# Kernel tuning notes

Measured on AMD Instinct MI355X. Metric: run time of the kernel, lower is better.

Reference implementation:

```python
import jax, jax.numpy as jnp
import numpy as np

N, E, F, R, L, B = 50000, 800000, 64, 20, 2, 64
RC = 5.0
ZMAX = 100
LN2 = 0.6931471805599453

def ssp(x):
    # shifted softplus: softplus(x) - log(2)
    return jax.nn.softplus(x) - LN2

def setup_inputs() -> dict:
    key = jax.random.key(0)
    ks = jax.random.split(key, 32)
    w = lambda i, shape: jax.random.normal(ks[i], shape, dtype=jnp.float32) * 0.05
    inp = {
        'z': jax.random.randint(ks[0], (N,), 0, ZMAX + 1),
        'pos': jax.random.normal(ks[1], (N, 3), dtype=jnp.float32) * 3.0,
        'edge_index': jax.random.randint(ks[2], (2, E), 0, N),
        'batch_idx': jnp.sort(jax.random.randint(ks[3], (N,), 0, B)),
        'emb': jax.random.normal(ks[4], (ZMAX + 1, F), dtype=jnp.float32),
        'phi_W': w(5, (L, 3 * F, F)), 'phi_b': w(6, (L, 3 * F)),
        'filt_W1': w(7, (L, F, R)), 'filt_b1': w(8, (L, F)),
        'filt_W2': w(9, (L, 3 * F, F)), 'filt_b2': w(10, (L, 3 * F)),
        'U_W': w(11, (L, F, F)), 'V_W': w(12, (L, F, F)),
        'a_W1': w(13, (L, F, 2 * F)), 'a_b1': w(14, (L, F)),
        'a_W2': w(15, (L, 3 * F, F)), 'a_b2': w(16, (L, 3 * F)),
        'e_W1': w(17, (F // 2, F)), 'e_b1': w(18, (F // 2,)),
        'e_W2': w(19, (1, F // 2)), 'e_b2': w(20, (1,)),
        'dip_w': w(21, (F,)),
    }
    return inp

def reference(z, pos, edge_index, batch_idx, emb, phi_W, phi_b,
              filt_W1, filt_b1, filt_W2, filt_b2, U_W, V_W,
              a_W1, a_b1, a_W2, a_b2, e_W1, e_b1, e_W2, e_b2, dip_w):
    src, dst = edge_index[0], edge_index[1]
    s = emb[z]                               # (N, F)
    v = jnp.zeros((N, F, 3), dtype=s.dtype)  # (N, F, 3)

    # edge geometry
    r_vec = pos[dst] - pos[src]              # (E, 3)
    r_norm = jnp.linalg.norm(r_vec, axis=-1)
    r_hat = r_vec / jnp.maximum(r_norm, 1e-8)[:, None]
    # Gaussian RBF on [0, RC], widths = grid spacing
    mu = jnp.linspace(0.0, RC, R, dtype=s.dtype)
    width = mu[1] - mu[0]
    e_ij = jnp.exp(-((r_norm[:, None] - mu[None, :]) ** 2) / (2.0 * width * width))
    fc = 0.5 * (jnp.cos(jnp.pi * r_norm / RC) + 1.0) * (r_norm < RC)
    e_ij = e_ij * fc[:, None]                # (E, R)

    for l in range(L):
        # message block
        filt = ssp(e_ij @ filt_W1[l].T + filt_b1[l]) @ filt_W2[l].T + filt_b2[l]  # (E, 3F)
        W_s, W_v, W_r = jnp.split(filt, 3, axis=-1)
        phi = s[dst] @ phi_W[l].T + phi_b[l]                                       # (E, 3F)
        phi_s, phi_v, phi_r = jnp.split(phi, 3, axis=-1)
        m_s = W_s * phi_s                                                          # (E, F)
        m_v = W_v[:, :, None] * v[dst] + (W_r * phi_r)[:, :, None] * r_hat[:, None, :]  # (E, F, 3)
        s = s + jax.ops.segment_sum(m_s, src, num_segments=N)
        v = v + jax.ops.segment_sum(m_v, src, num_segments=N)
        # update block
        Uv = jnp.einsum('nfd,gf->ngd', v, U_W[l])
        Vv = jnp.einsum('nfd,gf->ngd', v, V_W[l])
        Vv_norm_sq = jnp.sum(Vv * Vv, axis=-1)                                     # (N, F)
        a = ssp(jnp.concatenate([s, Vv_norm_sq], axis=-1) @ a_W1[l].T + a_b1[l]) @ a_W2[l].T + a_b2[l]
        a_ss, a_sv, a_vv = jnp.split(a, 3, axis=-1)
        inner = jnp.sum(Uv * Vv, axis=-1)
        s = s + a_ss + a_sv * inner
        v = v + a_vv[:, :, None] * Uv

    # heads
    eps_i = (ssp(s @ e_W1.T + e_b1) @ e_W2.T + e_b2)[:, 0]  # (N,)
    energy = jax.ops.segment_sum(eps_i, batch_idx, num_segments=B)
    mu_i = jnp.sum(v * dip_w[None, :, None], axis=1)         # (N, 3)
    mu_mol = jax.ops.segment_sum(mu_i, batch_idx, num_segments=B)
    dipole = jnp.linalg.norm(mu_mol, axis=-1)
    charges = jnp.zeros((N,), dtype=s.dtype)
    return energy, dipole, charges
```

## Files before the change

### kernel.cpp

```cpp
#include <hip/hip_runtime.h>
#include <math.h>

static constexpr int N  = 50000;
static constexpr int E  = 800000;
static constexpr int F  = 64;
static constexpr int R  = 20;
static constexpr int NL = 2;
static constexpr int B  = 64;
static constexpr float RC   = 5.0f;
static constexpr float LN2F = 0.6931471805599453f;
static constexpr float WIDTH  = RC / (R - 1);
static constexpr float INV2W2 = 1.0f / (2.0f * WIDTH * WIDTH);
static constexpr float PI_F = 3.14159265358979323846f;

static constexpr int   NB     = 4096;
static constexpr float DR     = RC / NB;
static constexpr float INV_DR = NB / RC;
static constexpr int   TROWS  = NB + 2;
static constexpr int   TENT   = NB + 1;

static constexpr int NBLK_SCAN = (N + 255) / 256;

typedef __attribute__((ext_vector_type(8))) short bf16x8;
typedef __attribute__((ext_vector_type(4))) float f32x4;
typedef __attribute__((ext_vector_type(3))) unsigned uint32x3;

__device__ __forceinline__ float ssp_f(float x) {
    return fmaxf(x, 0.0f) + log1pf(__expf(-fabsf(x))) - LN2F;
}

__device__ __forceinline__ short f2bf(float x) {
    unsigned u = __builtin_bit_cast(unsigned, x);
    unsigned r = (u + 0x7fffu + ((u >> 16) & 1u)) >> 16;
    return (short)r;
}
__device__ __forceinline__ float bf_lo(unsigned u) {
    return __builtin_bit_cast(float, u << 16);
}
__device__ __forceinline__ float bf_hi(unsigned u) {
    return __builtin_bit_cast(float, u & 0xffff0000u);
}

__global__ void k_hist(const int* __restrict__ ei, int* __restrict__ cnt) {
    int e = blockIdx.x * blockDim.x + threadIdx.x;
    if (e < E) atomicAdd(&cnt[ei[e]], 1);
}

__global__ void k_scan_a(const int* __restrict__ cnt, int* __restrict__ bsum) {
    __shared__ int part[256];
    const int t = threadIdx.x;
    const int idx = blockIdx.x * 256 + t;
    int v = (idx < N) ? cnt[idx] : 0;
    part[t] = v;
    __syncthreads();
    for (int d = 1; d < 256; d <<= 1) {
        int x = (t >= d) ? part[t - d] : 0;
        __syncthreads();
        part[t] += x;
        __syncthreads();
    }
    if (t == 255) bsum[blockIdx.x] = part[255];
}

__global__ void k_scan_b(const int* __restrict__ bsum, int* __restrict__ bpre,
                         int* __restrict__ offN) {
    __shared__ int part[256];
    const int t = threadIdx.x;
    int v = (t < NBLK_SCAN) ? bsum[t] : 0;
    part[t] = v;
    __syncthreads();
    for (int d = 1; d < 256; d <<= 1) {
        int x = (t >= d) ? part[t - d] : 0;
        __syncthreads();
        part[t] += x;
        __syncthreads();
    }
    if (t < NBLK_SCAN) bpre[t] = part[t] - v;
    if (t == NBLK_SCAN - 1) *offN = part[t];
}

__global__ void k_scan_c(const int* __restrict__ cnt, const int* __restrict__ bpre,
                         int* __restrict__ off, int* __restrict__ cur) {
    __shared__ int part[256];
    const int t = threadIdx.x;
    const int idx = blockIdx.x * 256 + t;
    int v = (idx < N) ? cnt[idx] : 0;
    part[t] = v;
    __syncthreads();
    for (int d = 1; d < 256; d <<= 1) {
        int x = (t >= d) ? part[t - d] : 0;
        __syncthreads();
        part[t] += x;
        __syncthreads();
    }
    if (idx < N) {
        int e = bpre[blockIdx.x] + part[t] - v;
        off[idx] = e;
        cur[idx] = e;
    }
}

__global__ void k_scatter(const int* __restrict__ ei, int* __restrict__ cur,
                          const float* __restrict__ pos, uint4* __restrict__ edata) {
    int e = blockIdx.x * blockDim.x + threadIdx.x;
    if (e >= E) return;
    int src = ei[e], dst = ei[E + e];
    int p = atomicAdd(&cur[src], 1);
    float qx = pos[dst * 3 + 0] - pos[src * 3 + 0];
    float qy = pos[dst * 3 + 1] - pos[src * 3 + 1];
    float qz = pos[dst * 3 + 2] - pos[src * 3 + 2];
    float rn = sqrtf(qx * qx + qy * qy + qz * qz);
    float invn = 1.0f / fmaxf(rn, 1e-8f);
    float t = rn * INV_DR;
    int i = (int)t;
    float fr = t - (float)i;
    if (i >= NB) { i = NB; fr = 0.0f; }
    uint4 rec;
    rec.x = (unsigned)dst;
    rec.y = (unsigned)i | ((unsigned)(unsigned short)f2bf(fr) << 16);
    rec.z = (unsigned)(unsigned short)f2bf(qx * invn)
          | ((unsigned)(unsigned short)f2bf(qy * invn) << 16);
    rec.w = (unsigned)(unsigned short)f2bf(qz * invn);
    edata[p] = rec;
}

__global__ void k_table(const float* __restrict__ fW1, const float* __restrict__ fb1,
                        const float* __restrict__ fW2, const float* __restrict__ fb2,
                        unsigned short* __restrict__ Tp) {
    const int l   = blockIdx.x / TROWS;
    const int row = blockIdx.x % TROWS;
    const int lane = threadIdx.x;
    const float r = fminf((float)row, (float)NB) * DR;
    const float fc = (r < RC) ? 0.5f * (__cosf(PI_F * r * (1.0f / RC)) + 1.0f) : 0.0f;

    __shared__ float sh[F];
    float acc = fb1[l * F + lane];
    const float* w1 = fW1 + (size_t)l * F * R + (size_t)lane * R;
    #pragma unroll
    for (int rr = 0; rr < R; rr++) {
        float dmu = r - rr * WIDTH;
        float er = __expf(-dmu * dmu * INV2W2) * fc;
        acc = fmaf(er, w1[rr], acc);
    }
    sh[lane] = ssp_f(acc);
    __syncthreads();
    unsigned short* TpL = Tp + (size_t)l * TENT * 384;
    #pragma unroll
    for (int p = 0; p < 3; p++) {
        int c = p * 64 + lane;
        float a = fb2[l * 192 + c];
        const float* w2 = fW2 + ((size_t)l * 192 + c) * 64;
        #pragma unroll 8
        for (int k = 0; k < F; k++) a = fmaf(sh[k], w2[k], a);
        unsigned short bf = (unsigned short)f2bf(a);
        if (row <= NB) TpL[(size_t)row * 384 + lane * 6 + p * 2 + 0] = bf;
        if (row >= 1)  TpL[(size_t)(row - 1) * 384 + lane * 6 + p * 2 + 1] = bf;
    }
}

__launch_bounds__(256)
__global__ void k_pack0(float* __restrict__ s, const int* __restrict__ z,
                        const float* __restrict__ emb,
                        const float* __restrict__ PW, const float* __restrict__ Pb,
                        unsigned* __restrict__ ndAV) {
    __shared__ float sbuf[4][F];
    const int lane = threadIdx.x & 63;
    const int wid  = threadIdx.x >> 6;
    const int gwave = blockIdx.x * 4 + wid;
    const int nwaves = gridDim.x * 4;

    float wsr[F], wrr[F];
    {
        const float* rs = PW + (size_t)lane * 64;
        const float* rr = PW + (size_t)(128 + lane) * 64;
        #pragma unroll
        for (int k = 0; k < F; k += 4) {
            float4 a = *(const float4*)(rs + k);
            wsr[k] = a.x; wsr[k+1] = a.y; wsr[k+2] = a.z; wsr[k+3] = a.w;
            float4 b = *(const float4*)(rr + k);
            wrr[k] = b.x; wrr[k+1] = b.y; wrr[k+2] = b.z; wrr[k+3] = b.w;
        }
    }
    const float bs = Pb[lane], br = Pb[128 + lane];

    for (int n = gwave; n < N; n += nwaves) {
        float sv = emb[(size_t)z[n] * F + lane];
        s[(size_t)n * F + lane] = sv;
        sbuf[wid][lane] = sv;
        float as = bs, ar = br;
        #pragma unroll
        for (int k = 0; k < F; k += 4) {
            float4 s4 = *(const float4*)&sbuf[wid][k];
            as = fmaf(s4.x, wsr[k],   as); as = fmaf(s4.y, wsr[k+1], as);
            as = fmaf(s4.z, wsr[k+2], as); as = fmaf(s4.w, wsr[k+3], as);
            ar = fmaf(s4.x, wrr[k],   ar); ar = fmaf(s4.y, wrr[k+1], ar);
            ar = fmaf(s4.z, wrr[k+2], ar); ar = fmaf(s4.w, wrr[k+3], ar);
        }
        ndAV[((size_t)n * 64 + lane) * 3] =
              (unsigned)(unsigned short)f2bf(as)
            | ((unsigned)(unsigned short)f2bf(ar) << 16);
    }
}

__device__ __forceinline__ uint32x3 load_tbl(const unsigned short* __restrict__ TpL,
                                             unsigned edy, int lane) {
    const int i = (int)(edy & 0xffffu);
    return *(const uint32x3*)(TpL + (size_t)i * 384 + lane * 6);
}

template<bool ACCUMV>
__device__ __forceinline__ uint32x3 load_rec(const unsigned* __restrict__ ndAV,
                                             unsigned dst, int lane) {
    const unsigned* p = ndAV + ((size_t)dst * 64 + lane) * 3;
    uint32x3 r;
    if (ACCUMV) {
        r = *(const uint32x3*)p;
    } else {
        r.x = *p; r.y = 0; r.z = 0;
    }
    return r;
}

template<bool ACCUMV>
__device__ __forceinline__ void consume_edge(const uint4 ed, const uint32x3 t,
                                             const uint32x3 r,
                                             float& ms, float& mv0, float& mv1, float& mv2) {
    const float fr = bf_hi(ed.y);
    const float Ws = fmaf(fr, bf_hi(t.x) - bf_lo(t.x), bf_lo(t.x));
    const float Wr = fmaf(fr, bf_hi(t.z) - bf_lo(t.z), bf_lo(t.z));
    ms = fmaf(Ws, bf_lo(r.x), ms);
    const float c = Wr * bf_hi(r.x);
    const float rhx = bf_lo(ed.z), rhy = bf_hi(ed.z), rhz = bf_lo(ed.w);
    if (ACCUMV) {
        const float Wv = fmaf(fr, bf_hi(t.y) - bf_lo(t.y), bf_lo(t.y));
        mv0 = fmaf(Wv, bf_lo(r.y), fmaf(c, rhx, mv0));
        mv1 = fmaf(Wv, bf_hi(r.y), fmaf(c, rhy, mv1));
        mv2 = fmaf(Wv, bf_lo(r.z), fmaf(c, rhz, mv2));
    } else {
        mv0 = fmaf(c, rhx, mv0);
        mv1 = fmaf(c, rhy, mv1);
        mv2 = fmaf(c, rhz, mv2);
    }
}

template<bool ACCUMV>
__launch_bounds__(256, 8)
__global__ void k_gather(const uint4* __restrict__ edata, const int* __restrict__ off,
                         const unsigned short* __restrict__ TpL,
                         const unsigned* __restrict__ ndAV,
                         float* __restrict__ s, float* __restrict__ v) {
    __shared__ float red[4][4][64];
    const int lane = threadIdx.x & 63;
    const int wv   = threadIdx.x >> 6;
    const int n = blockIdx.x;
    const int base = off[n], end = off[n + 1];

    float ms = 0.f, mv0 = 0.f, mv1 = 0.f, mv2 = 0.f;
    int kc = base + wv;
    if (kc < end) {
        uint4 edC = edata[kc];
        int kn = kc + 4;
        bool hasN = kn < end;
        uint4 edN = edC;
        if (hasN) edN = edata[kn];
        uint32x3 tC = load_tbl(TpL, edC.y, lane);
        uint32x3 rC = load_rec<ACCUMV>(ndAV, edC.x, lane);
        for (;;) {
            const int kn2 = kn + 4;
            const bool hasN2 = hasN && (kn2 < end);
            uint4 edN2 = edC;
            if (hasN2) edN2 = edata[kn2];
            uint32x3 tN = tC, rN = rC;
            if (hasN) {
                tN = load_tbl(TpL, edN.y, lane);
                rN = load_rec<ACCUMV>(ndAV, edN.x, lane);
            }
            consume_edge<ACCUMV>(edC, tC, rC, ms, mv0, mv1, mv2);
            if (!hasN) break;
            edC = edN; tC = tN; rC = rN;
            edN = edN2; hasN = hasN2; kn = kn2;
        }
    }
    red[wv][0][lane] = ms;
    red[wv][1][lane] = mv0;
    red[wv][2][lane] = mv1;
    red[wv][3][lane] = mv2;
    __syncthreads();
    if (wv == 0) {
        ms  = red[0][0][lane] + red[1][0][lane] + red[2][0][lane] + red[3][0][lane];
        mv0 = red[0][1][lane] + red[1][1][lane] + red[2][1][lane] + red[3][1][lane];
        mv1 = red[0][2][lane] + red[1][2][lane] + red[2][2][lane] + red[3][2][lane];
        mv2 = red[0][3][lane] + red[1][3][lane] + red[2][3][lane] + red[3][3][lane];
        s[(size_t)n * F + lane] += ms;
        float* vo = v + (size_t)n * 3 * F + lane;
        if (ACCUMV) {
            vo[0]     += mv0;
            vo[F]     += mv1;
            vo[2 * F] += mv2;
        } else {
            vo[0] = mv0; vo[F] = mv1; vo[2 * F] = mv2;
        }
    }
}

__device__ __forceinline__ bf16x8 load_wfrag(const float* __restrict__ Wp, int ldk,
                                             int nrow, int k0) {
    const float* p = Wp + (size_t)nrow * ldk + k0;
    float4 a = *(const float4*)p;
    float4 b = *(const float4*)(p + 4);
    bf16x8 r;
    r[0] = f2bf(a.x); r[1] = f2bf(a.y); r[2] = f2bf(a.z); r[3] = f2bf(a.w);
    r[4] = f2bf(b.x); r[5] = f2bf(b.y); r[6] = f2bf(b.z); r[7] = f2bf(b.w);
    return r;
}

template<bool DO_PACK>
__launch_bounds__(256)
__global__ void k_update_mfma(float* __restrict__ s, float* __restrict__ v,
                              const float* __restrict__ U_W, const float* __restrict__ V_W,
                              const float* __restrict__ aW1, const float* __restrict__ ab1,
                              const float* __restrict__ aW2, const float* __restrict__ ab2,
                              const float* __restrict__ PW, const float* __restrict__ Pb,
                              unsigned* __restrict__ ndAV) {
    __shared__ short vlds[96 * 72];
    __shared__ short xlds[32 * 136];
    __shared__ short hlds[32 * 72];

    const int tid = threadIdx.x;
    const int l   = tid & 63;
    const int w   = tid >> 6;
    const int lo  = l & 15;
    const int hi  = l >> 4;

    bf16x8 ufr[2], vfr[2], w1fr[4], w2fr[3][2];
    #pragma unroll
    for (int kk = 0; kk < 2; kk++) {
        ufr[kk] = load_wfrag(U_W, 64, w * 16 + lo, kk * 32 + hi * 8);
        vfr[kk] = load_wfrag(V_W, 64, w * 16 + lo, kk * 32 + hi * 8);
    }
    #pragma unroll
    for (int kk = 0; kk < 4; kk++)
        w1fr[kk] = load_wfrag(aW1, 128, w * 16 + lo, kk * 32 + hi * 8);
    #pragma unroll
    for (int p = 0; p < 3; p++)
        #pragma unroll
        for (int kk = 0; kk < 2; kk++)
            w2fr[p][kk] = load_wfrag(aW2, 64, p * 64 + w * 16 + lo, kk * 32 + hi * 8);

    bf16x8 pws[2], pwr[2];
    float pbs = 0.f, pbr = 0.f;
    if (DO_PACK) {
        #pragma unroll
        for (int kk = 0; kk < 2; kk++) {
            pws[kk] = load_wfrag(PW, 64, w * 16 + lo, kk * 32 + hi * 8);
            pwr[kk] = load_wfrag(PW, 64, 128 + w * 16 + lo, kk * 32 + hi * 8);
        }
        pbs = Pb[w * 16 + lo];
        pbr = Pb[128 + w * 16 + lo];
    }

    const float ab1c  = ab1[w * 16 + lo];
    const float ab2c0 = ab2[w * 16 + lo];
    const float ab2c1 = ab2[64 + w * 16 + lo];
    const float ab2c2 = ab2[128 + w * 16 + lo];
    const int g = w * 16 + lo;

    for (int half = 0; half < 2; half++) {
        const int n0 = blockIdx.x * 64 + half * 32;
        if (half) __syncthreads();

        for (int u = tid; u < 96 * 8; u += 256) {
            int row = u >> 3, oct = u & 7;
            int d = row >> 5, nn = row & 31;
            int n = min(n0 + nn, N - 1);
            const float* src = v + ((size_t)n * 3 + d) * 64 + oct * 8;
            float4 a = *(const float4*)src;
            float4 b = *(const float4*)(src + 4);
            bf16x8 t;
            t[0] = f2bf(a.x); t[1] = f2bf(a.y); t[2] = f2bf(a.z); t[3] = f2bf(a.w);
            t[4] = f2bf(b.x); t[5] = f2bf(b.y); t[6] = f2bf(b.z); t[7] = f2bf(b.w);
            *(bf16x8*)&vlds[row * 72 + oct * 8] = t;
        }
        for (int u = tid; u < 32 * 8; u += 256) {
            int nn = u >> 3, oct = u & 7;
            int n = min(n0 + nn, N - 1);
            const float* src = s + (size_t)n * 64 + oct * 8;
            float4 a = *(const float4*)src;
            float4 b = *(const float4*)(src + 4);
            bf16x8 t;
            t[0] = f2bf(a.x); t[1] = f2bf(a.y); t[2] = f2bf(a.z); t[3] = f2bf(a.w);
            t[4] = f2bf(b.x); t[5] = f2bf(b.y); t[6] = f2bf(b.z); t[7] = f2bf(b.w);
            *(bf16x8*)&xlds[nn * 136 + oct * 8] = t;
        }
        __syncthreads();

        f32x4 cu[6], cv[6];
        #pragma unroll
        for (int mt = 0; mt < 6; mt++) { cu[mt] = (f32x4)0.0f; cv[mt] = (f32x4)0.0f; }
        #pragma unroll
        for (int kk = 0; kk < 2; kk++) {
            #pragma unroll
            for (int mt = 0; mt < 6; mt++) {
                bf16x8 af = *(const bf16x8*)&vlds[(mt * 16 + lo) * 72 + kk * 32 + hi * 8];
                cu[mt] = __builtin_amdgcn_mfma_f32_16x16x32_bf16(af, ufr[kk], cu[mt], 0, 0, 0);
                cv[mt] = __builtin_amdgcn_mfma_f32_16x16x32_bf16(af, vfr[kk], cv[mt], 0, 0, 0);
            }
        }

        f32x4 inn[2];
        #pragma unroll
        for (int nt = 0; nt < 2; nt++) {
            #pragma unroll
            for (int r = 0; r < 4; r++) {
                float vs = 0.f, ii = 0.f;
                #pragma unroll
                for (int d = 0; d < 3; d++) {
                    float a = cu[d * 2 + nt][r], b = cv[d * 2 + nt][r];
                    vs = fmaf(b, b, vs);
                    ii = fmaf(a, b, ii);
                }
                inn[nt][r] = ii;
                int nl = nt * 16 + hi * 4 + r;
                xlds[nl * 136 + 64 + w * 16 + lo] = f2bf(vs);
            }
        }
        __syncthreads();

        f32x4 c2[2];
        c2[0] = (f32x4)0.0f; c2[1] = (f32x4)0.0f;
        #pragma unroll
        for (int kk = 0; kk < 4; kk++) {
            #pragma unroll
            for (int mt = 0; mt < 2; mt++) {
                bf16x8 af = *(const bf16x8*)&xlds[(mt * 16 + lo) * 136 + kk * 32 + hi * 8];
                c2[mt] = __builtin_amdgcn_mfma_f32_16x16x32_bf16(af, w1fr[kk], c2[mt], 0, 0, 0);
            }
        }
        #pragma unroll
        for (int mt = 0; mt < 2; mt++)
            #pragma unroll
            for (int r = 0; r < 4; r++) {
                float hv = ssp_f(c2[mt][r] + ab1c);
                hlds[(mt * 16 + hi * 4 + r) * 72 + w * 16 + lo] = f2bf(hv);
            }
        __syncthreads();

        f32x4 c3[2][3];
        #pragma unroll
        for (int mt = 0; mt < 2; mt++)
            #pragma unroll
            for (int p = 0; p < 3; p++) c3[mt][p] = (f32x4)0.0f;
        #pragma unroll
        for (int kk = 0; kk < 2; kk++) {
            #pragma unroll
            for (int mt = 0; mt < 2; mt++) {
                bf16x8 af = *(const bf16x8*)&hlds[(mt * 16 + lo) * 72 + kk * 32 + hi * 8];
                #pragma unroll
                for (int p = 0; p < 3; p++)
                    c3[mt][p] = __builtin_amdgcn_mfma_f32_16x16x32_bf16(af, w2fr[p][kk], c3[mt][p], 0, 0, 0);
            }
        }

        float snew[2][4];
        #pragma unroll
        for (int mt = 0; mt < 2; mt++) {
            #pragma unroll
            for (int r = 0; r < 4; r++) {
                int n = n0 + mt * 16 + hi * 4 + r;
                if (n >= N) { snew[mt][r] = 0.f; continue; }
                float a_ss = c3[mt][0][r] + ab2c0;
                float a_sv = c3[mt][1][r] + ab2c1;
                float a_vv = c3[mt][2][r] + ab2c2;
                size_t si = (size_t)n * 64 + g;
                float sn = s[si] + a_ss + a_sv * inn[mt][r];
                s[si] = sn;
                snew[mt][r] = sn;
                float vn[3];
                #pragma unroll
                for (int d = 0; d < 3; d++) {
                    size_t vi = ((size_t)n * 3 + d) * 64 + g;
                    vn[d] = v[vi] + a_vv * cu[d * 2 + mt][r];
                    v[vi] = vn[d];
                }
                if (DO_PACK) {
                    unsigned* pp = ndAV + ((size_t)n * 64 + g) * 3;
                    pp[1] = (unsigned)(unsigned short)f2bf(vn[0])
                          | ((unsigned)(unsigned short)f2bf(vn[1]) << 16);
                    pp[2] = (unsigned)(unsigned short)f2bf(vn[2]);
                }
            }
        }

        if (DO_PACK) {
            __syncthreads();
            #pragma unroll
            for (int mt = 0; mt < 2; mt++)
                #pragma unroll
                for (int r = 0; r < 4; r++)
                    hlds[(mt * 16 + hi * 4 + r) * 72 + g] = f2bf(snew[mt][r]);
            __syncthreads();

            f32x4 cs[2], cr[2];
            cs[0] = (f32x4)0.0f; cs[1] = (f32x4)0.0f;
            cr[0] = (f32x4)0.0f; cr[1] = (f32x4)0.0f;
            #pragma unroll
            for (int kk = 0; kk < 2; kk++) {
                #pragma unroll
                for (int mt = 0; mt < 2; mt++) {
                    bf16x8 af = *(const bf16x8*)&hlds[(mt * 16 + lo) * 72 + kk * 32 + hi * 8];
                    cs[mt] = __builtin_amdgcn_mfma_f32_16x16x32_bf16(af, pws[kk], cs[mt], 0, 0, 0);
                    cr[mt] = __builtin_amdgcn_mfma_f32_16x16x32_bf16(af, pwr[kk], cr[mt], 0, 0, 0);
                }
            }
            #pragma unroll
            for (int mt = 0; mt < 2; mt++) {
                #pragma unroll
                for (int r = 0; r < 4; r++) {
                    int n = n0 + mt * 16 + hi * 4 + r;
                    if (n >= N) continue;
                    ndAV[((size_t)n * 64 + g) * 3] =
                          (unsigned)(unsigned short)f2bf(cs[mt][r] + pbs)
                        | ((unsigned)(unsigned short)f2bf(cr[mt][r] + pbr) << 16);
                }
            }
        }
    }
}

__global__ void k_heads(const float* __restrict__ s, const float* __restrict__ v,
                        const int* __restrict__ batch_idx,
                        const float* __restrict__ eW1, const float* __restrict__ eb1,
                        const float* __restrict__ eW2, const float* __restrict__ eb2,
                        const float* __restrict__ dip_w,
                        float* __restrict__ eacc, float* __restrict__ macc) {
    __shared__ float se[B];
    __shared__ float sm[3][B];
    if (threadIdx.x < B) se[threadIdx.x] = 0.0f;
    if (threadIdx.x < 3 * B) sm[threadIdx.x >> 6][threadIdx.x & 63] = 0.0f;
    __syncthreads();
    int n = blockIdx.x * blockDim.x + threadIdx.x;
    if (n < N) {
        int b = batch_idx[n];
        float sr[F];
        #pragma unroll
        for (int f = 0; f < F; f += 4) {
            float4 t = *(const float4*)&s[(size_t)n * F + f];
            sr[f] = t.x; sr[f+1] = t.y; sr[f+2] = t.z; sr[f+3] = t.w;
        }
        float eps = eb2[0];
        for (int jj = 0; jj < F / 2; jj++) {
            float acc = eb1[jj];
            #pragma unroll
            for (int f = 0; f < F; f++)
                acc = fmaf(sr[f], eW1[jj * F + f], acc);
            eps = fmaf(eW2[jj], ssp_f(acc), eps);
        }
        atomicAdd(&se[b], eps);
        #pragma unroll
        for (int d = 0; d < 3; d++) {
            float m = 0.0f;
            #pragma unroll 8
            for (int f = 0; f < F; f++)
                m = fmaf(v[((size_t)n * 3 + d) * F + f], dip_w[f], m);
            atomicAdd(&sm[d][b], m);
        }
    }
    __syncthreads();
    if (threadIdx.x < B) atomicAdd(&eacc[threadIdx.x], se[threadIdx.x]);
    if (threadIdx.x >= B && threadIdx.x < 4 * B) {
        int d = (threadIdx.x >> 6) - 1, b = threadIdx.x & 63;
        atomicAdd(&macc[d * B + b], sm[d][b]);
    }
}

__global__ void k_final(const float* __restrict__ eacc, const float* __restrict__ macc,
                        float* __restrict__ out) {
    int b = threadIdx.x;
    if (b < B) {
        out[b] = eacc[b];
        float mx = macc[b], my = macc[B + b], mz = macc[2 * B + b];
        out[B + b] = sqrtf(mx * mx + my * my + mz * mz);
    }
}

extern "C" void kernel_launch(void* const* d_in, const int* in_sizes, int n_in,
                              void* d_out, int out_size, void* d_ws, size_t ws_size,
                              hipStream_t stream) {
    const int*   z     = (const int*)d_in[0];
    const float* pos   = (const float*)d_in[1];
    const int*   ei    = (const int*)d_in[2];
    const int*   bidx  = (const int*)d_in[3];
    const float* emb   = (const float*)d_in[4];
    const float* phi_W = (const float*)d_in[5];
    const float* phi_b = (const float*)d_in[6];
    const float* fW1   = (const float*)d_in[7];
    const float* fb1   = (const float*)d_in[8];
    const float* fW2   = (const float*)d_in[9];
    const float* fb2   = (const float*)d_in[10];
    const float* U_W   = (const float*)d_in[11];
    const float* V_W   = (const float*)d_in[12];
    const float* aW1   = (const float*)d_in[13];
    const float* ab1   = (const float*)d_in[14];
    const float* aW2   = (const float*)d_in[15];
    const float* ab2   = (const float*)d_in[16];
    const float* eW1   = (const float*)d_in[17];
    const float* eb1   = (const float*)d_in[18];
    const float* eW2   = (const float*)d_in[19];
    const float* eb2   = (const float*)d_in[20];
    const float* dip_w = (const float*)d_in[21];
    float* out = (float*)d_out;

    float* ws = (float*)d_ws;
    float* s    = ws;
    float* v    = s + (size_t)N * F;
    unsigned* ndAV = (unsigned*)(v + (size_t)N * F * 3);
    unsigned short* Tp = (unsigned short*)(ndAV + (size_t)N * 64 * 3);
    float* eacc = (float*)(Tp + (size_t)NL * TENT * 384);
    float* macc = eacc + B;
    int*   cnt  = (int*)(macc + 3 * B);
    int*   off  = cnt  + N;
    int*   cur  = off  + N + 1;
    int*   bsum = cur  + N;
    int*   bpre = bsum + 256;
    uint4* edata = (uint4*)(((uintptr_t)(bpre + 256) + 15) & ~(uintptr_t)15);

    hipMemsetAsync(cnt,  0, sizeof(int) * N, stream);
    hipMemsetAsync(eacc, 0, sizeof(float) * 4 * B, stream);
    hipMemsetAsync(out + 2 * B, 0, sizeof(float) * (size_t)N, stream);

    k_hist<<<(E + 255) / 256, 256, 0, stream>>>(ei, cnt);
    k_scan_a<<<NBLK_SCAN, 256, 0, stream>>>(cnt, bsum);
    k_scan_b<<<1, 256, 0, stream>>>(bsum, bpre, off + N);
    k_scan_c<<<NBLK_SCAN, 256, 0, stream>>>(cnt, bpre, off, cur);
    k_scatter<<<(E + 255) / 256, 256, 0, stream>>>(ei, cur, pos, edata);
    k_table<<<NL * TROWS, 64, 0, stream>>>(fW1, fb1, fW2, fb2, Tp);

    const int ublocks = (N + 63) / 64;
    k_pack0<<<512, 256, 0, stream>>>(s, z, emb, phi_W, phi_b, ndAV);
    k_gather<false><<<N, 256, 0, stream>>>(edata, off, Tp, ndAV, s, v);
    k_update_mfma<true><<<ublocks, 256, 0, stream>>>(s, v,
        U_W, V_W, aW1, ab1, aW2, ab2,
        phi_W + (size_t)192 * 64, phi_b + 192, ndAV);
    k_gather<true><<<N, 256, 0, stream>>>(edata, off,
        Tp + (size_t)TENT * 384, ndAV, s, v);
    k_update_mfma<false><<<ublocks, 256, 0, stream>>>(s, v,
        U_W + 4096, V_W + 4096, aW1 + 8192, ab1 + F, aW2 + 12288, ab2 + 192,
        nullptr, nullptr, nullptr);

    k_heads<<<(N + 255) / 256, 256, 0, stream>>>(s, v, bidx, eW1, eb1, eW2, eb2,
                                                 dip_w, eacc, macc);
    k_final<<<1, 64, 0, stream>>>(eacc, macc, out);
}
```

Baseline: 540.7 us.

## Map one wave per node in gather with padded even edge segments

The gather kernel now gives each node to a single wave (four nodes per block) instead of splitting a node's edges over four waves and reducing through shared memory. The barrier and shared-memory reduction go away. CSR segments are padded to even length with dummy edges that point at a zero table row, so the software-pipelined loop can always prefetch two edges ahead. The layer-0 node record is also split into a compact dense array so the first gather reads 4 bytes per lane instead of striding over 12. The cost is less parallelism for high-degree nodes, a serial per-node edge loop, and extra padding edges to process.

```diff
diff --git a/kernel.cpp b/kernel.cpp
--- a/kernel.cpp
+++ b/kernel.cpp
@@ -17,7 +17,8 @@
 static constexpr float DR     = RC / NB;
 static constexpr float INV_DR = NB / RC;
 static constexpr int   TROWS  = NB + 2;
-static constexpr int   TENT   = NB + 1;
+static constexpr int   IZERO  = NB + 1;
+static constexpr int   TENTA  = NB + 2;
 
 static constexpr int NBLK_SCAN = (N + 255) / 256;
 
@@ -50,7 +51,7 @@
     __shared__ int part[256];
     const int t = threadIdx.x;
     const int idx = blockIdx.x * 256 + t;
-    int v = (idx < N) ? cnt[idx] : 0;
+    int v = (idx < N) ? ((cnt[idx] + 1) & ~1) : 0;
     part[t] = v;
     __syncthreads();
     for (int d = 1; d < 256; d <<= 1) {
@@ -80,11 +81,13 @@
 }
 
 __global__ void k_scan_c(const int* __restrict__ cnt, const int* __restrict__ bpre,
-                         int* __restrict__ off, int* __restrict__ cur) {
+                         int* __restrict__ off, int* __restrict__ cur,
+                         uint4* __restrict__ edata) {
     __shared__ int part[256];
     const int t = threadIdx.x;
     const int idx = blockIdx.x * 256 + t;
-    int v = (idx < N) ? cnt[idx] : 0;
+    int vraw = (idx < N) ? cnt[idx] : 0;
+    int v = (vraw + 1) & ~1;
     part[t] = v;
     __syncthreads();
     for (int d = 1; d < 256; d <<= 1) {
@@ -97,6 +100,13 @@
         int e = bpre[blockIdx.x] + part[t] - v;
         off[idx] = e;
         cur[idx] = e;
+        if (vraw & 1) {
+            uint4 nil;
+            nil.x = (unsigned)idx;
+            nil.y = (unsigned)IZERO;
+            nil.z = 0u; nil.w = 0u;
+            edata[e + vraw] = nil;
+        }
     }
 }
 
@@ -144,7 +154,7 @@
     }
     sh[lane] = ssp_f(acc);
     __syncthreads();
-    unsigned short* TpL = Tp + (size_t)l * TENT * 384;
+    unsigned short* TpL = Tp + (size_t)l * TENTA * 384;
     #pragma unroll
     for (int p = 0; p < 3; p++) {
         int c = p * 64 + lane;
@@ -156,13 +166,18 @@
         if (row <= NB) TpL[(size_t)row * 384 + lane * 6 + p * 2 + 0] = bf;
         if (row >= 1)  TpL[(size_t)(row - 1) * 384 + lane * 6 + p * 2 + 1] = bf;
     }
+    if (row == 0) {
+        #pragma unroll
+        for (int j = 0; j < 6; j++)
+            TpL[(size_t)IZERO * 384 + lane * 6 + j] = 0;
+    }
 }
 
 __launch_bounds__(256)
 __global__ void k_pack0(float* __restrict__ s, const int* __restrict__ z,
                         const float* __restrict__ emb,
                         const float* __restrict__ PW, const float* __restrict__ Pb,
-                        unsigned* __restrict__ ndAV) {
+                        unsigned* __restrict__ ndA0) {
     __shared__ float sbuf[4][F];
     const int lane = threadIdx.x & 63;
     const int wid  = threadIdx.x >> 6;
@@ -196,29 +211,9 @@
             ar = fmaf(s4.x, wrr[k],   ar); ar = fmaf(s4.y, wrr[k+1], ar);
             ar = fmaf(s4.z, wrr[k+2], ar); ar = fmaf(s4.w, wrr[k+3], ar);
         }
-        ndAV[((size_t)n * 64 + lane) * 3] =
-              (unsigned)(unsigned short)f2bf(as)
-            | ((unsigned)(unsigned short)f2bf(ar) << 16);
-    }
-}
-
-__device__ __forceinline__ uint32x3 load_tbl(const unsigned short* __restrict__ TpL,
-                                             unsigned edy, int lane) {
-    const int i = (int)(edy & 0xffffu);
-    return *(const uint32x3*)(TpL + (size_t)i * 384 + lane * 6);
-}
-
-template<bool ACCUMV>
-__device__ __forceinline__ uint32x3 load_rec(const unsigned* __restrict__ ndAV,
-                                             unsigned dst, int lane) {
-    const unsigned* p = ndAV + ((size_t)dst * 64 + lane) * 3;
-    uint32x3 r;
-    if (ACCUMV) {
-        r = *(const uint32x3*)p;
-    } else {
-        r.x = *p; r.y = 0; r.z = 0;
-    }
-    return r;
+        ndA0[(size_t)n * 64 + lane] = (unsigned)(unsigned short)f2bf(as)
+                                    | ((unsigned)(unsigned short)f2bf(ar) << 16);
+    }
 }
 
 template<bool ACCUMV>
@@ -247,59 +242,60 @@
 __launch_bounds__(256, 8)
 __global__ void k_gather(const uint4* __restrict__ edata, const int* __restrict__ off,
                          const unsigned short* __restrict__ TpL,
+                         const unsigned* __restrict__ ndA0,
                          const unsigned* __restrict__ ndAV,
                          float* __restrict__ s, float* __restrict__ v) {
-    __shared__ float red[4][4][64];
     const int lane = threadIdx.x & 63;
     const int wv   = threadIdx.x >> 6;
-    const int n = blockIdx.x;
+    const int n = blockIdx.x * 4 + wv;
+    if (n >= N) return;
     const int base = off[n], end = off[n + 1];
 
     float ms = 0.f, mv0 = 0.f, mv1 = 0.f, mv2 = 0.f;
-    int kc = base + wv;
-    if (kc < end) {
-        uint4 edC = edata[kc];
-        int kn = kc + 4;
-        bool hasN = kn < end;
-        uint4 edN = edC;
-        if (hasN) edN = edata[kn];
-        uint32x3 tC = load_tbl(TpL, edC.y, lane);
-        uint32x3 rC = load_rec<ACCUMV>(ndAV, edC.x, lane);
-        for (;;) {
-            const int kn2 = kn + 4;
-            const bool hasN2 = hasN && (kn2 < end);
-            uint4 edN2 = edC;
-            if (hasN2) edN2 = edata[kn2];
-            uint32x3 tN = tC, rN = rC;
-            if (hasN) {
-                tN = load_tbl(TpL, edN.y, lane);
-                rN = load_rec<ACCUMV>(ndAV, edN.x, lane);
-            }
-            consume_edge<ACCUMV>(edC, tC, rC, ms, mv0, mv1, mv2);
-            if (!hasN) break;
-            edC = edN; tC = tN; rC = rN;
-            edN = edN2; hasN = hasN2; kn = kn2;
-        }
-    }
-    red[wv][0][lane] = ms;
-    red[wv][1][lane] = mv0;
-    red[wv][2][lane] = mv1;
-    red[wv][3][lane] = mv2;
-    __syncthreads();
-    if (wv == 0) {
-        ms  = red[0][0][lane] + red[1][0][lane] + red[2][0][lane] + red[3][0][lane];
-        mv0 = red[0][1][lane] + red[1][1][lane] + red[2][1][lane] + red[3][1][lane];
-        mv1 = red[0][2][lane] + red[1][2][lane] + red[2][2][lane] + red[3][2][lane];
-        mv2 = red[0][3][lane] + red[1][3][lane] + red[2][3][lane] + red[3][3][lane];
-        s[(size_t)n * F + lane] += ms;
-        float* vo = v + (size_t)n * 3 * F + lane;
+
+    if (base < end) {
+        uint4 ed0 = edata[base];
+        uint4 ed1 = edata[base + 1];
+        uint32x3 t0 = *(const uint32x3*)(TpL + (size_t)(ed0.y & 0xffffu) * 384 + lane * 6);
+        uint32x3 r0;
         if (ACCUMV) {
-            vo[0]     += mv0;
-            vo[F]     += mv1;
-            vo[2 * F] += mv2;
+            r0 = *(const uint32x3*)(ndAV + ((size_t)ed0.x * 64 + lane) * 3);
         } else {
-            vo[0] = mv0; vo[F] = mv1; vo[2 * F] = mv2;
-        }
+            r0.x = ndA0[(size_t)ed0.x * 64 + lane]; r0.y = 0; r0.z = 0;
+        }
+
+        for (int k = base; k < end - 2; ++k) {
+            uint4 ed2 = edata[k + 2];
+            uint32x3 t1 = *(const uint32x3*)(TpL + (size_t)(ed1.y & 0xffffu) * 384 + lane * 6);
+            uint32x3 r1;
+            if (ACCUMV) {
+                r1 = *(const uint32x3*)(ndAV + ((size_t)ed1.x * 64 + lane) * 3);
+            } else {
+                r1.x = ndA0[(size_t)ed1.x * 64 + lane]; r1.y = 0; r1.z = 0;
+            }
+            consume_edge<ACCUMV>(ed0, t0, r0, ms, mv0, mv1, mv2);
+            ed0 = ed1; t0 = t1; r0 = r1;
+            ed1 = ed2;
+        }
+        uint32x3 t1 = *(const uint32x3*)(TpL + (size_t)(ed1.y & 0xffffu) * 384 + lane * 6);
+        uint32x3 r1;
+        if (ACCUMV) {
+            r1 = *(const uint32x3*)(ndAV + ((size_t)ed1.x * 64 + lane) * 3);
+        } else {
+            r1.x = ndA0[(size_t)ed1.x * 64 + lane]; r1.y = 0; r1.z = 0;
+        }
+        consume_edge<ACCUMV>(ed0, t0, r0, ms, mv0, mv1, mv2);
+        consume_edge<ACCUMV>(ed1, t1, r1, ms, mv0, mv1, mv2);
+    }
+
+    s[(size_t)n * F + lane] += ms;
+    float* vo = v + (size_t)n * 3 * F + lane;
+    if (ACCUMV) {
+        vo[0]     += mv0;
+        vo[F]     += mv1;
+        vo[2 * F] += mv2;
+    } else {
+        vo[0] = mv0; vo[F] = mv1; vo[2 * F] = mv2;
     }
 }
 
@@ -613,9 +609,10 @@
     float* ws = (float*)d_ws;
     float* s    = ws;
     float* v    = s + (size_t)N * F;
-    unsigned* ndAV = (unsigned*)(v + (size_t)N * F * 3);
+    unsigned* ndA0 = (unsigned*)(v + (size_t)N * F * 3);
+    unsigned* ndAV = ndA0 + (size_t)N * 64;
     unsigned short* Tp = (unsigned short*)(ndAV + (size_t)N * 64 * 3);
-    float* eacc = (float*)(Tp + (size_t)NL * TENT * 384);
+    float* eacc = (float*)(Tp + (size_t)NL * TENTA * 384);
     float* macc = eacc + B;
     int*   cnt  = (int*)(macc + 3 * B);
     int*   off  = cnt  + N;
@@ -631,18 +628,19 @@
     k_hist<<<(E + 255) / 256, 256, 0, stream>>>(ei, cnt);
     k_scan_a<<<NBLK_SCAN, 256, 0, stream>>>(cnt, bsum);
     k_scan_b<<<1, 256, 0, stream>>>(bsum, bpre, off + N);
-    k_scan_c<<<NBLK_SCAN, 256, 0, stream>>>(cnt, bpre, off, cur);
+    k_scan_c<<<NBLK_SCAN, 256, 0, stream>>>(cnt, bpre, off, cur, edata);
     k_scatter<<<(E + 255) / 256, 256, 0, stream>>>(ei, cur, pos, edata);
     k_table<<<NL * TROWS, 64, 0, stream>>>(fW1, fb1, fW2, fb2, Tp);
 
+    const int gblocks = (N + 3) / 4;
     const int ublocks = (N + 63) / 64;
-    k_pack0<<<512, 256, 0, stream>>>(s, z, emb, phi_W, phi_b, ndAV);
-    k_gather<false><<<N, 256, 0, stream>>>(edata, off, Tp, ndAV, s, v);
+    k_pack0<<<512, 256, 0, stream>>>(s, z, emb, phi_W, phi_b, ndA0);
+    k_gather<false><<<gblocks, 256, 0, stream>>>(edata, off, Tp, ndA0, ndAV, s, v);
     k_update_mfma<true><<<ublocks, 256, 0, stream>>>(s, v,
         U_W, V_W, aW1, ab1, aW2, ab2,
         phi_W + (size_t)192 * 64, phi_b + 192, ndAV);
-    k_gather<true><<<N, 256, 0, stream>>>(edata, off,
-        Tp + (size_t)TENT * 384, ndAV, s, v);
+    k_gather<true><<<gblocks, 256, 0, stream>>>(edata, off,
+        Tp + (size_t)TENTA * 384, ndA0, ndAV, s, v);
     k_update_mfma<false><<<ublocks, 256, 0, stream>>>(s, v,
         U_W + 4096, V_W + 4096, aW1 + 8192, ab1 + F, aW2 + 12288, ab2 + 192,
         nullptr, nullptr, nullptr);
```

Result: faster. 499.6 us (-7.6%).
